# Kernel tuning notes

Measured on AMD Instinct MI355X. Metric: run time of the kernel, lower is better.

Reference implementation:

```python
import jax, jax.numpy as jnp
import numpy as np

ALPHA = 0.2          # LeakyReLU negative slope
NEG_INF = -9e15      # mask value from the original code


def setup_inputs() -> dict:
    key = jax.random.key(0)
    k1, k2, k3, k4 = jax.random.split(key, 4)
    B, N, F_in, F_out = 8, 2048, 64, 64
    x = jax.random.normal(k1, (B, N, F_in), dtype=jnp.float32)
    adj = jax.random.randint(k2, (B, N, N), 0, 2, dtype=jnp.int32)
    W = jax.random.normal(k3, (F_in, F_out), dtype=jnp.float32)
    a = jax.random.normal(k4, (2 * F_out, 1), dtype=jnp.float32)
    return {"x": x, "adj": adj, "W": W, "a": a}


def reference(x, adj, W, a):
    # h: [B, N, F_out]
    h = jnp.matmul(x, W)
    F_out = W.shape[1]
    a1 = a[:F_out, 0]   # source half of attention vector
    a2 = a[F_out:, 0]   # target half
    # e_ij = leakyrelu(h_i . a1 + h_j . a2)  -- identical math to the
    # original cat([h_i, h_j]) @ a without materializing [B,N*N,2F].
    s1 = jnp.einsum('bnf,f->bn', h, a1)  # [B, N]
    s2 = jnp.einsum('bnf,f->bn', h, a2)  # [B, N]
    e = jax.nn.leaky_relu(s1[:, :, None] + s2[:, None, :], negative_slope=ALPHA)
    masked = jnp.where(adj > 0, e, NEG_INF)
    attention = jax.nn.softmax(masked, axis=2)  # [B, N, N]
    # dropout p=0.0 / eval mode -> identity
    h_prime = jnp.matmul(attention, h)          # [B, N, F_out]
    return jax.nn.elu(h_prime)                  # concat=True branch
```

## Files before the change

### kernel.cpp

```cpp
#include <hip/hip_runtime.h>
#include <cstdint>

#define LRELU_ALPHA 0.2f
#define NEG_INF -9000000000000000.0f
#define L2E 1.4426950408889634f

typedef __bf16 bf16x8 __attribute__((ext_vector_type(8)));
typedef unsigned short ushortx8 __attribute__((ext_vector_type(8)));
typedef float floatx4 __attribute__((ext_vector_type(4)));

constexpr int Bb = 8, Nn = 2048, Ff = 64;
constexpr int TJ = 64;
constexpr int LSTR = 72;
constexpr int SEG = 8;
constexpr int SEGT = (Nn / TJ) / SEG;
constexpr int NROWS = Bb * Nn;

__device__ __forceinline__ unsigned short f2bf(float f) {
    unsigned u = __builtin_bit_cast(unsigned, f);
    u = u + 0x7FFFu + ((u >> 16) & 1u);
    return (unsigned short)(u >> 16);
}

__global__ __launch_bounds__(256) void gat_prep(
    const float* __restrict__ x, const float* __restrict__ W, const float* __restrict__ a,
    unsigned short* __restrict__ hT, float* __restrict__ s1g, float* __restrict__ s2g)
{
    constexpr int STR2 = 36;
    __shared__ unsigned short hblk[64 * STR2];
    const int tid = threadIdx.x;
    const int blk = blockIdx.x;
    const int b  = blk >> 6;
    const int i0 = (blk & 63) * 32;
    const int w    = tid >> 6;
    const int lane = tid & 63;

    float wcol[64];
    #pragma unroll
    for (int k = 0; k < 64; ++k) wcol[k] = W[k * 64 + lane];
    const float a1 = a[lane], a2 = a[64 + lane];

    for (int r = 0; r < 8; ++r) {
        const int il = w * 8 + r;
        const int i  = i0 + il;
        const float* xrow = x + ((size_t)(b * Nn + i)) * 64;
        float h = 0.f;
        #pragma unroll
        for (int k = 0; k < 64; ++k) h = fmaf(xrow[k], wcol[k], h);
        float p1 = h * a1, p2 = h * a2;
        #pragma unroll
        for (int off = 32; off; off >>= 1) {
            p1 += __shfl_xor(p1, off);
            p2 += __shfl_xor(p2, off);
        }
        if (lane == 0) { s1g[b * Nn + i] = p1; s2g[b * Nn + i] = p2; }
        hblk[lane * STR2 + il] = f2bf(h);
    }
    __syncthreads();
    {
        const int f = tid >> 2, c = (tid & 3) * 8;
        uint4 v = *reinterpret_cast<const uint4*>(&hblk[f * STR2 + c]);
        *reinterpret_cast<uint4*>(hT + ((size_t)b * 64 + f) * Nn + i0 + c) = v;
    }
}

__global__ __launch_bounds__(128) void gat_attn(
    const int* __restrict__ adj, const unsigned short* __restrict__ hT,
    const float* __restrict__ s1g, const float* __restrict__ s2g,
    float* __restrict__ m_part, float* __restrict__ l_part, float* __restrict__ O_part)
{
    __shared__ unsigned short hT_lds[64 * LSTR];
    __shared__ float s2_lds[TJ];

    const int tid  = threadIdx.x;
    const int blk  = blockIdx.x;
    const int seg  = blk >> 9;
    const int grp  = blk & 511;
    const int gr0  = grp * 32;
    const int b    = gr0 >> 11;
    const int i0   = gr0 & 2047;
    const int w    = tid >> 6;
    const int lane = tid & 63;
    const int fl   = lane & 15;
    const int q    = lane >> 4;

    const int i = i0 + w * 16 + fl;
    const float s1v = s1g[b * Nn + i];
    const int* adj_row = adj + ((size_t)(b * Nn + i)) * Nn;
    const unsigned short* hTb = hT + (size_t)b * 64 * Nn;
    const float* s2b = s2g + b * Nn;

    float m = NEG_INF, l = 0.f;
    floatx4 C[4] = {};

    const int sf = tid >> 1, sc = (tid & 1) * 32;

    const int jt0 = seg * SEGT;

    int4 adjv[4];
    {
        const int* arow = adj_row + jt0 * TJ;
        const int4* ap0 = reinterpret_cast<const int4*>(arow + q * 8);
        adjv[0] = ap0[0]; adjv[1] = ap0[1];
        const int4* ap1 = reinterpret_cast<const int4*>(arow + 32 + q * 8);
        adjv[2] = ap1[0]; adjv[3] = ap1[1];
    }

    for (int jt = jt0; jt < jt0 + SEGT; ++jt) {
        const int j0 = jt * TJ;
        __syncthreads();
        {
            const uint4* gsrc = reinterpret_cast<const uint4*>(hTb + (size_t)sf * Nn + j0 + sc);
            uint4 g0 = gsrc[0], g1 = gsrc[1], g2 = gsrc[2], g3 = gsrc[3];
            uint4* ldst = reinterpret_cast<uint4*>(&hT_lds[sf * LSTR + sc]);
            ldst[0] = g0; ldst[1] = g1; ldst[2] = g2; ldst[3] = g3;
            if (tid < TJ) s2_lds[tid] = s2b[j0 + tid];
        }
        __syncthreads();

        int4 nadj[4] = {};
        if (jt + 1 < jt0 + SEGT) {
            const int* nrow = adj_row + j0 + TJ;
            const int4* ap0 = reinterpret_cast<const int4*>(nrow + q * 8);
            nadj[0] = ap0[0]; nadj[1] = ap0[1];
            const int4* ap1 = reinterpret_cast<const int4*>(nrow + 32 + q * 8);
            nadj[2] = ap1[0]; nadj[3] = ap1[1];
        }

        float e[16];
        const int* av = reinterpret_cast<const int*>(adjv);
        #pragma unroll
        for (int t = 0; t < 2; ++t) {
            float s2v[8];
            *reinterpret_cast<float4*>(&s2v[0]) =
                *reinterpret_cast<const float4*>(&s2_lds[t * 32 + q * 8]);
            *reinterpret_cast<float4*>(&s2v[4]) =
                *reinterpret_cast<const float4*>(&s2_lds[t * 32 + q * 8 + 4]);
            #pragma unroll
            for (int jj = 0; jj < 8; ++jj) {
                float ev = s1v + s2v[jj];
                ev = fmaxf(ev, LRELU_ALPHA * ev);
                e[t * 8 + jj] = (av[t * 8 + jj] > 0) ? ev : NEG_INF;
            }
        }
        float tmax = e[0];
        #pragma unroll
        for (int k = 1; k < 16; ++k) tmax = fmaxf(tmax, e[k]);
        tmax = fmaxf(tmax, __shfl_xor(tmax, 16));
        tmax = fmaxf(tmax, __shfl_xor(tmax, 32));
        const float m_new = fmaxf(m, tmax);
        const float alpha_s = exp2f((m - m_new) * L2E);
        m = m_new;

        float tsum = 0.f;
        float p[16];
        #pragma unroll
        for (int k = 0; k < 16; ++k) {
            p[k] = exp2f((e[k] - m_new) * L2E);
            tsum += p[k];
        }
        tsum += __shfl_xor(tsum, 16);
        tsum += __shfl_xor(tsum, 32);
        l = l * alpha_s + tsum;

        ushortx8 a0v, a1v;
#if __has_builtin(__builtin_amdgcn_cvt_pk_bf16_f32)
        #pragma unroll
        for (int jj = 0; jj < 4; ++jj) {
            ushortx8* dst = jj < 2 ? &a0v : &a1v;
        }
        #pragma unroll
        for (int jj = 0; jj < 8; ++jj) { a0v[jj] = f2bf(p[jj]); a1v[jj] = f2bf(p[8 + jj]); }
#else
        #pragma unroll
        for (int jj = 0; jj < 8; ++jj) { a0v[jj] = f2bf(p[jj]); a1v[jj] = f2bf(p[8 + jj]); }
#endif
        const bf16x8 A0 = __builtin_bit_cast(bf16x8, a0v);
        const bf16x8 A1 = __builtin_bit_cast(bf16x8, a1v);

        float ac[4];
        #pragma unroll
        for (int r = 0; r < 4; ++r) ac[r] = __shfl(alpha_s, q * 4 + r);
        #pragma unroll
        for (int u = 0; u < 4; ++u)
            #pragma unroll
            for (int r = 0; r < 4; ++r) C[u][r] *= ac[r];

        #pragma unroll
        for (int u = 0; u < 4; ++u) {
            const bf16x8 B0 = *reinterpret_cast<const bf16x8*>(
                &hT_lds[(u * 16 + fl) * LSTR + q * 8]);
            C[u] = __builtin_amdgcn_mfma_f32_16x16x32_bf16(A0, B0, C[u], 0, 0, 0);
            const bf16x8 B1 = *reinterpret_cast<const bf16x8*>(
                &hT_lds[(u * 16 + fl) * LSTR + 32 + q * 8]);
            C[u] = __builtin_amdgcn_mfma_f32_16x16x32_bf16(A1, B1, C[u], 0, 0, 0);
        }
        adjv[0] = nadj[0]; adjv[1] = nadj[1]; adjv[2] = nadj[2]; adjv[3] = nadj[3];
    }

    if (q == 0) {
        const int ri = b * Nn + i;
        m_part[seg * NROWS + ri] = m;
        l_part[seg * NROWS + ri] = l;
    }
    #pragma unroll
    for (int u = 0; u < 4; ++u) {
        #pragma unroll
        for (int r = 0; r < 4; ++r) {
            const int orow = i0 + w * 16 + q * 4 + r;
            O_part[((size_t)seg * NROWS + b * Nn + orow) * 64 + u * 16 + fl] = C[u][r];
        }
    }
}

__global__ __launch_bounds__(256) void gat_merge(
    const float* __restrict__ m_part, const float* __restrict__ l_part,
    const float* __restrict__ O_part, float* __restrict__ out)
{
    const int tid = threadIdx.x;
    const int ri  = blockIdx.x * 4 + (tid >> 6);
    const int f   = tid & 63;

    float mv[SEG];
    #pragma unroll
    for (int s = 0; s < SEG; ++s) mv[s] = m_part[s * NROWS + ri];
    float mstar = mv[0];
    #pragma unroll
    for (int s = 1; s < SEG; ++s) mstar = fmaxf(mstar, mv[s]);

    float lsum = 0.f, acc = 0.f;
    #pragma unroll
    for (int s = 0; s < SEG; ++s) {
        const float wgt = exp2f((mv[s] - mstar) * L2E);
        lsum += l_part[s * NROWS + ri] * wgt;
        acc  += O_part[((size_t)s * NROWS + ri) * 64 + f] * wgt;
    }
    float v = acc / lsum;
    v = (v > 0.f) ? v : (exp2f(v * L2E) - 1.f);
    out[(size_t)ri * 64 + f] = v;
}

extern "C" void kernel_launch(void* const* d_in, const int* in_sizes, int n_in,
                              void* d_out, int out_size, void* d_ws, size_t ws_size,
                              hipStream_t stream) {
    const float* x   = (const float*)d_in[0];
    const int*   adj = (const int*)d_in[1];
    const float* W   = (const float*)d_in[2];
    const float* a   = (const float*)d_in[3];
    float* out = (float*)d_out;

    char* p = (char*)d_ws;
    unsigned short* hT = (unsigned short*)p;  p += (size_t)Bb * 64 * Nn * sizeof(unsigned short);
    float* s1 = (float*)p;                    p += (size_t)NROWS * sizeof(float);
    float* s2 = (float*)p;                    p += (size_t)NROWS * sizeof(float);
    float* m_part = (float*)p;                p += (size_t)SEG * NROWS * sizeof(float);
    float* l_part = (float*)p;                p += (size_t)SEG * NROWS * sizeof(float);
    float* O_part = (float*)p;

    gat_prep<<<dim3(Bb * Nn / 32), dim3(256), 0, stream>>>(x, W, a, hT, s1, s2);
    gat_attn<<<dim3(SEG * (Bb * Nn / 32)), dim3(128), 0, stream>>>(
        adj, hT, s1, s2, m_part, l_part, O_part);
    gat_merge<<<dim3(NROWS / 4), dim3(256), 0, stream>>>(m_part, l_part, O_part, out);
}
```

Before: 237.9 us.

## Load whole segment of hT into LDS once, 256-thread blocks, prescale scores by log2e

Each attention block now covers 64 rows with 256 threads and loads the entire 256-column hT segment and s2 slice into LDS in one go. This removes the per-tile __syncthreads pairs and reloads, and the four tiles are unrolled with double-buffered adjacency prefetch. The scores are premultiplied by log2(e) in the prep kernel, which drops multiplies in the exponentials and in merge, and bf16 packing is done two values at a time. The trade-off is more LDS per block (about 34KB) and higher register pressure, which could lower occupancy.

```diff
diff --git a/kernel.cpp b/kernel.cpp
--- a/kernel.cpp
+++ b/kernel.cpp
@@ -6,20 +6,27 @@
 #define L2E 1.4426950408889634f
 
 typedef __bf16 bf16x8 __attribute__((ext_vector_type(8)));
-typedef unsigned short ushortx8 __attribute__((ext_vector_type(8)));
 typedef float floatx4 __attribute__((ext_vector_type(4)));
 
 constexpr int Bb = 8, Nn = 2048, Ff = 64;
 constexpr int TJ = 64;
-constexpr int LSTR = 72;
 constexpr int SEG = 8;
-constexpr int SEGT = (Nn / TJ) / SEG;
+constexpr int SEGJ = Nn / SEG;
+constexpr int SEGT = SEGJ / TJ;
 constexpr int NROWS = Bb * Nn;
+constexpr int LSTR = 264;
+
+__device__ __forceinline__ unsigned f2bf_u(float f) {
+    unsigned u = __builtin_bit_cast(unsigned, f);
+    return u + 0x7FFFu + ((u >> 16) & 1u);
+}
 
 __device__ __forceinline__ unsigned short f2bf(float f) {
-    unsigned u = __builtin_bit_cast(unsigned, f);
-    u = u + 0x7FFFu + ((u >> 16) & 1u);
-    return (unsigned short)(u >> 16);
+    return (unsigned short)(f2bf_u(f) >> 16);
+}
+
+__device__ __forceinline__ unsigned pkbf(float lo, float hi) {
+    return (f2bf_u(lo) >> 16) | (f2bf_u(hi) & 0xFFFF0000u);
 }
 
 __global__ __launch_bounds__(256) void gat_prep(
@@ -53,7 +60,7 @@
             p1 += __shfl_xor(p1, off);
             p2 += __shfl_xor(p2, off);
         }
-        if (lane == 0) { s1g[b * Nn + i] = p1; s2g[b * Nn + i] = p2; }
+        if (lane == 0) { s1g[b * Nn + i] = p1 * L2E; s2g[b * Nn + i] = p2 * L2E; }
         hblk[lane * STR2 + il] = f2bf(h);
     }
     __syncthreads();
@@ -64,19 +71,19 @@
     }
 }
 
-__global__ __launch_bounds__(128) void gat_attn(
+__global__ __launch_bounds__(256, 4) void gat_attn(
     const int* __restrict__ adj, const unsigned short* __restrict__ hT,
     const float* __restrict__ s1g, const float* __restrict__ s2g,
     float* __restrict__ m_part, float* __restrict__ l_part, float* __restrict__ O_part)
 {
     __shared__ unsigned short hT_lds[64 * LSTR];
-    __shared__ float s2_lds[TJ];
+    __shared__ float s2_lds[SEGJ];
 
     const int tid  = threadIdx.x;
     const int blk  = blockIdx.x;
-    const int seg  = blk >> 9;
-    const int grp  = blk & 511;
-    const int gr0  = grp * 32;
+    const int seg  = blk >> 8;
+    const int grp  = blk & 255;
+    const int gr0  = grp * 64;
     const int b    = gr0 >> 11;
     const int i0   = gr0 & 2047;
     const int w    = tid >> 6;
@@ -88,54 +95,47 @@
     const float s1v = s1g[b * Nn + i];
     const int* adj_row = adj + ((size_t)(b * Nn + i)) * Nn;
     const unsigned short* hTb = hT + (size_t)b * 64 * Nn;
-    const float* s2b = s2g + b * Nn;
+    const int jseg0 = seg * SEGJ;
 
     float m = NEG_INF, l = 0.f;
     floatx4 C[4] = {};
 
-    const int sf = tid >> 1, sc = (tid & 1) * 32;
-
-    const int jt0 = seg * SEGT;
-
-    int4 adjv[4];
+    auto loadAdj = [&](int4* dst, int jcol0) {
+        const int* p0 = adj_row + jcol0 + q * 8;
+        dst[0] = *reinterpret_cast<const int4*>(p0);
+        dst[1] = *reinterpret_cast<const int4*>(p0 + 4);
+        const int* p1 = adj_row + jcol0 + 32 + q * 8;
+        dst[2] = *reinterpret_cast<const int4*>(p1);
+        dst[3] = *reinterpret_cast<const int4*>(p1 + 4);
+    };
+
+    int4 bufA[4], bufB[4];
+    loadAdj(bufA, jseg0);
+    loadAdj(bufB, jseg0 + TJ);
+
     {
-        const int* arow = adj_row + jt0 * TJ;
-        const int4* ap0 = reinterpret_cast<const int4*>(arow + q * 8);
-        adjv[0] = ap0[0]; adjv[1] = ap0[1];
-        const int4* ap1 = reinterpret_cast<const int4*>(arow + 32 + q * 8);
-        adjv[2] = ap1[0]; adjv[3] = ap1[1];
-    }
-
-    for (int jt = jt0; jt < jt0 + SEGT; ++jt) {
-        const int j0 = jt * TJ;
-        __syncthreads();
-        {
-            const uint4* gsrc = reinterpret_cast<const uint4*>(hTb + (size_t)sf * Nn + j0 + sc);
-            uint4 g0 = gsrc[0], g1 = gsrc[1], g2 = gsrc[2], g3 = gsrc[3];
-            uint4* ldst = reinterpret_cast<uint4*>(&hT_lds[sf * LSTR + sc]);
-            ldst[0] = g0; ldst[1] = g1; ldst[2] = g2; ldst[3] = g3;
-            if (tid < TJ) s2_lds[tid] = s2b[j0 + tid];
-        }
-        __syncthreads();
-
-        int4 nadj[4] = {};
-        if (jt + 1 < jt0 + SEGT) {
-            const int* nrow = adj_row + j0 + TJ;
-            const int4* ap0 = reinterpret_cast<const int4*>(nrow + q * 8);
-            nadj[0] = ap0[0]; nadj[1] = ap0[1];
-            const int4* ap1 = reinterpret_cast<const int4*>(nrow + 32 + q * 8);
-            nadj[2] = ap1[0]; nadj[3] = ap1[1];
-        }
-
+        const int fr = tid >> 2;
+        const int c0 = (tid & 3) * 64;
+        const unsigned short* gsrc = hTb + (size_t)fr * Nn + jseg0 + c0;
+        #pragma unroll
+        for (int k = 0; k < 8; ++k) {
+            uint4 v = reinterpret_cast<const uint4*>(gsrc)[k];
+            reinterpret_cast<uint4*>(&hT_lds[fr * LSTR + c0])[k] = v;
+        }
+        s2_lds[tid] = s2g[b * Nn + jseg0 + tid];
+    }
+    __syncthreads();
+
+    auto tile_body = [&](const int4* av4, int tloc) {
+        const int* av = reinterpret_cast<const int*>(av4);
         float e[16];
-        const int* av = reinterpret_cast<const int*>(adjv);
         #pragma unroll
         for (int t = 0; t < 2; ++t) {
             float s2v[8];
             *reinterpret_cast<float4*>(&s2v[0]) =
-                *reinterpret_cast<const float4*>(&s2_lds[t * 32 + q * 8]);
+                *reinterpret_cast<const float4*>(&s2_lds[tloc * 64 + t * 32 + q * 8]);
             *reinterpret_cast<float4*>(&s2v[4]) =
-                *reinterpret_cast<const float4*>(&s2_lds[t * 32 + q * 8 + 4]);
+                *reinterpret_cast<const float4*>(&s2_lds[tloc * 64 + t * 32 + q * 8 + 4]);
             #pragma unroll
             for (int jj = 0; jj < 8; ++jj) {
                 float ev = s1v + s2v[jj];
@@ -149,34 +149,26 @@
         tmax = fmaxf(tmax, __shfl_xor(tmax, 16));
         tmax = fmaxf(tmax, __shfl_xor(tmax, 32));
         const float m_new = fmaxf(m, tmax);
-        const float alpha_s = exp2f((m - m_new) * L2E);
+        const float alpha_s = exp2f(m - m_new);
         m = m_new;
 
-        float tsum = 0.f;
-        float p[16];
+        float tsum = 0.f, p[16];
         #pragma unroll
         for (int k = 0; k < 16; ++k) {
-            p[k] = exp2f((e[k] - m_new) * L2E);
+            p[k] = exp2f(e[k] - m_new);
             tsum += p[k];
         }
         tsum += __shfl_xor(tsum, 16);
         tsum += __shfl_xor(tsum, 32);
         l = l * alpha_s + tsum;
 
-        ushortx8 a0v, a1v;
-#if __has_builtin(__builtin_amdgcn_cvt_pk_bf16_f32)
-        #pragma unroll
-        for (int jj = 0; jj < 4; ++jj) {
-            ushortx8* dst = jj < 2 ? &a0v : &a1v;
-        }
-        #pragma unroll
-        for (int jj = 0; jj < 8; ++jj) { a0v[jj] = f2bf(p[jj]); a1v[jj] = f2bf(p[8 + jj]); }
-#else
-        #pragma unroll
-        for (int jj = 0; jj < 8; ++jj) { a0v[jj] = f2bf(p[jj]); a1v[jj] = f2bf(p[8 + jj]); }
-#endif
-        const bf16x8 A0 = __builtin_bit_cast(bf16x8, a0v);
-        const bf16x8 A1 = __builtin_bit_cast(bf16x8, a1v);
+        uint4 pl0, pl1;
+        pl0.x = pkbf(p[0], p[1]);  pl0.y = pkbf(p[2], p[3]);
+        pl0.z = pkbf(p[4], p[5]);  pl0.w = pkbf(p[6], p[7]);
+        pl1.x = pkbf(p[8], p[9]);  pl1.y = pkbf(p[10], p[11]);
+        pl1.z = pkbf(p[12], p[13]); pl1.w = pkbf(p[14], p[15]);
+        const bf16x8 A0 = __builtin_bit_cast(bf16x8, pl0);
+        const bf16x8 A1 = __builtin_bit_cast(bf16x8, pl1);
 
         float ac[4];
         #pragma unroll
@@ -189,14 +181,20 @@
         #pragma unroll
         for (int u = 0; u < 4; ++u) {
             const bf16x8 B0 = *reinterpret_cast<const bf16x8*>(
-                &hT_lds[(u * 16 + fl) * LSTR + q * 8]);
+                &hT_lds[(u * 16 + fl) * LSTR + tloc * 64 + q * 8]);
             C[u] = __builtin_amdgcn_mfma_f32_16x16x32_bf16(A0, B0, C[u], 0, 0, 0);
             const bf16x8 B1 = *reinterpret_cast<const bf16x8*>(
-                &hT_lds[(u * 16 + fl) * LSTR + 32 + q * 8]);
+                &hT_lds[(u * 16 + fl) * LSTR + tloc * 64 + 32 + q * 8]);
             C[u] = __builtin_amdgcn_mfma_f32_16x16x32_bf16(A1, B1, C[u], 0, 0, 0);
         }
-        adjv[0] = nadj[0]; adjv[1] = nadj[1]; adjv[2] = nadj[2]; adjv[3] = nadj[3];
-    }
+    };
+
+    tile_body(bufA, 0);
+    loadAdj(bufA, jseg0 + 2 * TJ);
+    tile_body(bufB, 1);
+    loadAdj(bufB, jseg0 + 3 * TJ);
+    tile_body(bufA, 2);
+    tile_body(bufB, 3);
 
     if (q == 0) {
         const int ri = b * Nn + i;
@@ -231,7 +229,7 @@
     float lsum = 0.f, acc = 0.f;
     #pragma unroll
     for (int s = 0; s < SEG; ++s) {
-        const float wgt = exp2f((mv[s] - mstar) * L2E);
+        const float wgt = exp2f(mv[s] - mstar);
         lsum += l_part[s * NROWS + ri] * wgt;
         acc  += O_part[((size_t)s * NROWS + ri) * 64 + f] * wgt;
     }
@@ -258,7 +256,7 @@
     float* O_part = (float*)p;
 
     gat_prep<<<dim3(Bb * Nn / 32), dim3(256), 0, stream>>>(x, W, a, hT, s1, s2);
-    gat_attn<<<dim3(SEG * (Bb * Nn / 32)), dim3(128), 0, stream>>>(
+    gat_attn<<<dim3(SEG * (Bb * Nn / 64)), dim3(256), 0, stream>>>(
         adj, hT, s1, s2, m_part, l_part, O_part);
     gat_merge<<<dim3(NROWS / 4), dim3(256), 0, stream>>>(m_part, l_part, O_part, out);
 }
```

Result: no change. 238.0 us (+0.1%).
